# Performance work log

Measured on AMD Instinct MI355X. Metric: run time of the kernel, lower is better.

The kernel has to match this reference:

```python
import jax, jax.numpy as jnp
import numpy as np

NP_, NG_ = 20000, 5000            # protein / go_annotation node counts
D_FEAT, D_HID, N_CLS = 512, 128, 1000
E_PP, E_PG, E_GP = 240000, 100000, 100000
NEG_SLOPE = -0.2                  # note: the repo default slope is negative
EPS = 1e-12


def _l2norm(x):
    n = jnp.linalg.norm(x, axis=1, keepdims=True)
    return x / jnp.maximum(n, EPS)


def _edge_softmax(logits, dst, n):
    # per-destination-node softmax over incoming edges, per feature channel
    m = jax.ops.segment_max(logits, dst, num_segments=n)
    e = jnp.exp(logits - m[dst])
    s = jax.ops.segment_sum(e, dst, num_segments=n)
    return e / s[dst]


def _type_attn(h_src, h_dst, src, dst, Wl, bl, Wr, br):
    # GCN-normalized aggregation onto dst nodes, then type-level attention logits,
    # broadcast back to edges (copy_u on the reversed relation graph).
    ns, nd = h_src.shape[0], h_dst.shape[0]
    ones = jnp.ones(src.shape[0], dtype=h_src.dtype)
    outdeg = jnp.clip(jax.ops.segment_sum(ones, src, num_segments=ns), 1.0)
    feat = h_src * (outdeg ** -0.5)[:, None]
    rst = jax.ops.segment_sum(feat[src], dst, num_segments=nd)
    indeg = jnp.clip(jax.ops.segment_sum(ones, dst, num_segments=nd), 1.0)
    rst = rst * (indeg ** -0.5)[:, None]
    ea = jax.nn.elu((h_dst @ Wl + bl) + (rst @ Wr + br))  # [nd, D_HID]
    return ea[dst]                                        # [E, D_HID]


def setup_inputs() -> dict:
    key = jax.random.key(0)
    ks = iter(jax.random.split(key, 40))

    def nrm(shape, s=0.05):
        return jax.random.normal(next(ks), shape, dtype=jnp.float32) * s

    def ri(n, hi):
        return jax.random.randint(next(ks), (n,), 0, hi, dtype=jnp.int32)

    zeros = lambda n: jnp.zeros((n,), jnp.float32)
    return dict(
        x_protein=jax.random.normal(next(ks), (NP_, D_FEAT), dtype=jnp.float32),
        x_go=jax.random.normal(next(ks), (NG_, N_CLS), dtype=jnp.float32),
        src_pp=ri(E_PP, NP_), dst_pp=ri(E_PP, NP_),
        src_pg=ri(E_PG, NP_), dst_pg=ri(E_PG, NG_),
        src_gp=ri(E_GP, NG_), dst_gp=ri(E_GP, NP_),
        W1p=nrm((D_FEAT, D_HID)), b1p=zeros(D_HID),
        W1g=nrm((N_CLS, D_HID)), b1g=zeros(D_HID),
        Wl_p=nrm((D_HID, D_HID)), bl_p=zeros(D_HID),
        Wl_g=nrm((D_HID, D_HID)), bl_g=zeros(D_HID),
        Wr_p=nrm((D_HID, D_HID)), br_p=zeros(D_HID),
        Wr_g=nrm((D_HID, D_HID)), br_g=zeros(D_HID),
        Wnl=nrm((D_HID, D_HID)), bnl=zeros(D_HID),
        Wnr=nrm((D_HID, D_HID)), bnr=zeros(D_HID),
        Wfc=nrm((D_HID, N_CLS)), bfc=zeros(N_CLS),
    )


def reference(x_protein, x_go, src_pp, dst_pp, src_pg, dst_pg, src_gp, dst_gp,
              W1p, b1p, W1g, b1g, Wl_p, bl_p, Wl_g, bl_g,
              Wr_p, br_p, Wr_g, br_g, Wnl, bnl, Wnr, bnr, Wfc, bfc):
    # input projection + row-wise l2 norm (dropout disabled / eval mode)
    hp = _l2norm(x_protein @ W1p + b1p)   # [NP, D_HID]
    hg = _l2norm(x_go @ W1g + b1g)        # [NG, D_HID]

    # ---- TypeAttention over each canonical etype ----
    a_pp = _type_attn(hp, hp, src_pp, dst_pp, Wl_p, bl_p, Wr_p, br_p)
    a_pg = _type_attn(hp, hg, src_pg, dst_pg, Wl_g, bl_g, Wr_p, br_p)
    a_gp = _type_attn(hg, hp, src_gp, dst_gp, Wl_p, bl_p, Wr_g, br_g)

    # homogeneous view: proteins [0,NP), go_annotation [NP,NP+NG)
    gsrc = jnp.concatenate([src_pp, src_pg, src_gp + NP_])
    gdst = jnp.concatenate([dst_pp, dst_pg + NP_, dst_gp])
    alpha = jnp.concatenate([a_pp, a_pg, a_gp], axis=0)   # [E, D_HID]
    n = NP_ + NG_
    alpha = _edge_softmax(alpha, gdst, n)

    # ---- NodeAttention on the homogeneous graph ----
    x = jnp.concatenate([hp, hg], axis=0)                 # [N, D_HID]
    hl = (x @ Wnl + bnl)[gsrc]
    hr = (x @ Wnr + bnr)[gdst]
    e = (hl + hr) * alpha
    e = jnp.where(e > 0, e, NEG_SLOPE * e)                # LeakyReLU(slope=-0.2)
    a = _edge_softmax(e, gdst, n)
    h = jax.ops.segment_sum(x[gsrc] * a, gdst, num_segments=n)

    out = h @ Wfc + bfc   # [N, N_CLS]; rows [:NP]=protein, [NP:]=go_annotation
    return out
```

## Files before the change

### kernel.cpp

```cpp
#include <hip/hip_runtime.h>
#include <math.h>

#define NP 20000
#define NG 5000
#define NTOT 25000
#define DF 512
#define NCLS 1000
#define DH 128
#define EPP 240000
#define EPG 100000
#define EGP 100000
#define ETOT 440000
#define FS 16
#define HB 16

typedef __attribute__((ext_vector_type(8))) __bf16 bf16x8;
typedef __attribute__((ext_vector_type(4))) float f32x4;

__device__ __forceinline__ void gl2lds16(const void* g, void* l) {
    __builtin_amdgcn_global_load_lds(
        (const __attribute__((address_space(1))) unsigned int*)g,
        (__attribute__((address_space(3))) unsigned int*)l, 16, 0, 0);
}

__device__ __forceinline__ float b2f(unsigned short u) {
    union { unsigned int i; float f; } c; c.i = ((unsigned int)u) << 16; return c.f;
}

__global__ __launch_bounds__(1024) void hist_part_kernel(
    const int* __restrict__ src_pp, const int* __restrict__ dst_pp,
    const int* __restrict__ src_pg, const int* __restrict__ dst_pg,
    const int* __restrict__ src_gp, const int* __restrict__ dst_gp,
    int* __restrict__ partial)
{
    __shared__ int bins[20000];
    const int job = blockIdx.y, b = blockIdx.x;
    const int* idx; int nbins, nedge; size_t pbase;
    switch (job) {
    case 0: idx = src_pp; nbins = 20000; nedge = EPP; pbase = 0;       break;
    case 1: idx = dst_pp; nbins = 20000; nedge = EPP; pbase = 320000;  break;
    case 2: idx = src_pg; nbins = 20000; nedge = EPG; pbase = 640000;  break;
    case 3: idx = dst_pg; nbins = 5000;  nedge = EPG; pbase = 960000;  break;
    case 4: idx = src_gp; nbins = 5000;  nedge = EGP; pbase = 1040000; break;
    default: idx = dst_gp; nbins = 20000; nedge = EGP; pbase = 1120000; break;
    }
    for (int i = threadIdx.x; i < nbins; i += 1024) bins[i] = 0;
    __syncthreads();
    const int chunk = (nedge + HB - 1) / HB;
    const int e0 = b * chunk, e1 = min(e0 + chunk, nedge);
    for (int e = e0 + threadIdx.x; e < e1; e += 1024) atomicAdd(&bins[idx[e]], 1);
    __syncthreads();
    int* dst = partial + pbase + (size_t)b * nbins;
    for (int i = threadIdx.x; i < nbins; i += 1024) dst[i] = bins[i];
}

__global__ __launch_bounds__(256) void hist_merge_kernel(const int* __restrict__ partial,
    int* __restrict__ outdeg_pp, int* __restrict__ indeg_pp,
    int* __restrict__ outdeg_pg, int* __restrict__ indeg_pg,
    int* __restrict__ outdeg_gp, int* __restrict__ indeg_gp)
{
    const int job = blockIdx.y;
    const int nbins = (job == 3 || job == 4) ? 5000 : 20000;
    const int bin = blockIdx.x * 256 + threadIdx.x;
    if (bin >= nbins) return;
    size_t pbase; int* outp;
    switch (job) {
    case 0: pbase = 0;       outp = outdeg_pp; break;
    case 1: pbase = 320000;  outp = indeg_pp;  break;
    case 2: pbase = 640000;  outp = outdeg_pg; break;
    case 3: pbase = 960000;  outp = indeg_pg;  break;
    case 4: pbase = 1040000; outp = outdeg_gp; break;
    default: pbase = 1120000; outp = indeg_gp; break;
    }
    const int* p = partial + pbase + bin;
    int s = 0;
#pragma unroll
    for (int b = 0; b < HB; b++) s += p[(size_t)b * nbins];
    outp[bin] = s;
}

__global__ __launch_bounds__(1024) void scan_kernel(const int* __restrict__ indeg_pp,
                                                    const int* __restrict__ indeg_gp,
                                                    const int* __restrict__ indeg_pg,
                                                    int* __restrict__ row_ptr)
{
    __shared__ int part[1024];
    int t = threadIdx.x;
    const int CH = (NTOT + 1023) / 1024;
    int base = t * CH;
    auto cntf = [&](int idx) -> int {
        return (idx < NP) ? (indeg_pp[idx] + indeg_gp[idx]) : indeg_pg[idx - NP];
    };
    int s = 0;
    for (int i = 0; i < CH; i++) { int idx = base + i; if (idx < NTOT) s += cntf(idx); }
    part[t] = s;
    __syncthreads();
    for (int off = 1; off < 1024; off <<= 1) {
        int v = (t >= off) ? part[t - off] : 0;
        __syncthreads();
        part[t] += v;
        __syncthreads();
    }
    int run = (t == 0) ? 0 : part[t - 1];
    for (int i = 0; i < CH; i++) {
        int idx = base + i;
        if (idx < NTOT) { row_ptr[idx] = run; run += cntf(idx); }
    }
    if (t == 1023) row_ptr[NTOT] = part[1023];
}

__global__ void scatter_kernel(const int* __restrict__ src_pp, const int* __restrict__ dst_pp,
                               const int* __restrict__ src_pg, const int* __restrict__ dst_pg,
                               const int* __restrict__ src_gp, const int* __restrict__ dst_gp,
                               const int* __restrict__ outdeg_pp, const int* __restrict__ outdeg_pg,
                               const int* __restrict__ outdeg_gp,
                               const int* __restrict__ row_ptr, int* fill,
                               int2* __restrict__ edata)
{
    int e = blockIdx.x * blockDim.x + threadIdx.x;
    int s, d, t; float sc;
    if (e < EPP) {
        s = src_pp[e]; d = dst_pp[e]; t = 0;
        sc = rsqrtf((float)max(outdeg_pp[s], 1));
    } else if (e < EPP + EPG) {
        int i = e - EPP; s = src_pg[i]; d = NP + dst_pg[i]; t = 1;
        sc = rsqrtf((float)max(outdeg_pg[s], 1));
    } else if (e < ETOT) {
        int i = e - EPP - EPG; int sl = src_gp[i]; s = NP + sl; d = dst_gp[i]; t = 2;
        sc = rsqrtf((float)max(outdeg_gp[sl], 1));
    } else return;
    int pos = row_ptr[d] + atomicAdd(&fill[d * FS], 1);
    edata[pos] = make_int2(s | (t << 16), __float_as_int(sc));
}

__global__ __launch_bounds__(256) void conv_x_kernel(const float* __restrict__ xp, const float* __restrict__ xg,
                                                     __bf16* __restrict__ xpb, __bf16* __restrict__ xgb)
{
    long long e = ((long long)blockIdx.x * 256 + threadIdx.x) * 8;
    __bf16 pk[8];
    if (blockIdx.y == 0) {
        if (e >= (long long)20032 * 512) return;
        int row = (int)(e >> 9), k = (int)(e & 511);
        if (row < NP) {
            f32x4 v0 = *(const f32x4*)(xp + (size_t)row * 512 + k);
            f32x4 v1 = *(const f32x4*)(xp + (size_t)row * 512 + k + 4);
#pragma unroll
            for (int i = 0; i < 4; i++) { pk[i] = (__bf16)v0[i]; pk[4 + i] = (__bf16)v1[i]; }
        } else {
#pragma unroll
            for (int i = 0; i < 8; i++) pk[i] = (__bf16)0.f;
        }
        *(bf16x8*)(xpb + e) = *(bf16x8*)pk;
    } else {
        if (e >= (long long)5056 * 1024) return;
        int row = (int)(e >> 10), k = (int)(e & 1023);
        if (row < NG && k + 7 < 1000) {
            f32x4 v0 = *(const f32x4*)(xg + (size_t)row * 1000 + k);
            f32x4 v1 = *(const f32x4*)(xg + (size_t)row * 1000 + k + 4);
#pragma unroll
            for (int i = 0; i < 4; i++) { pk[i] = (__bf16)v0[i]; pk[4 + i] = (__bf16)v1[i]; }
        } else {
#pragma unroll
            for (int i = 0; i < 8; i++) {
                int kk = k + i;
                pk[i] = (__bf16)((row < NG && kk < 1000) ? xg[(size_t)row * 1000 + kk] : 0.f);
            }
        }
        *(bf16x8*)(xgb + e) = *(bf16x8*)pk;
    }
}

__global__ __launch_bounds__(256) void conv_w_kernel(
    const float* W1p, const float* W1g, const float* Wlp, const float* Wrp, const float* Wrg,
    const float* Wnl, const float* Wnr, const float* Wfc,
    __bf16* w1pt, __bf16* w1gt, __bf16* wlpt, __bf16* wrpt, __bf16* wrgt,
    __bf16* wnlt, __bf16* wnrt, __bf16* wfct)
{
    int e = blockIdx.x * 256 + threadIdx.x;
    switch (blockIdx.y) {
    case 0: if (e < 128 * 512)  { int n = e >> 9, k = e & 511;  w1pt[e] = (__bf16)W1p[(size_t)k * 128 + n]; } break;
    case 1: if (e < 128 * 1024) { int n = e >> 10, k = e & 1023; w1gt[e] = (__bf16)(k < 1000 ? W1g[(size_t)k * 128 + n] : 0.f); } break;
    case 2: if (e < 16384) { int n = e >> 7, k = e & 127; wlpt[e] = (__bf16)Wlp[(size_t)k * 128 + n]; } break;
    case 3: if (e < 16384) { int n = e >> 7, k = e & 127; wrpt[e] = (__bf16)Wrp[(size_t)k * 128 + n]; } break;
    case 4: if (e < 16384) { int n = e >> 7, k = e & 127; wrgt[e] = (__bf16)Wrg[(size_t)k * 128 + n]; } break;
    case 5: if (e < 16384) { int n = e >> 7, k = e & 127; wnlt[e] = (__bf16)Wnl[(size_t)k * 128 + n]; } break;
    case 6: if (e < 16384) { int n = e >> 7, k = e & 127; wnrt[e] = (__bf16)Wnr[(size_t)k * 128 + n]; } break;
    case 7: if (e < 1024 * 128) { int n = e >> 7, k = e & 127; wfct[e] = (__bf16)(n < 1000 ? Wfc[(size_t)k * 1000 + n] : 0.f); } break;
    }
}

struct GJob {
    const __bf16* A1;
    const __bf16* B1; const __bf16* B2;
    const float* b1; const float* b2;
    float* O1; __bf16* O2; __bf16* Ob;
    int M, N, Kp, ksteps;
};

template<int ACT, int DUALW, int EMIT>
__global__ __launch_bounds__(256) void gemm_bt(GJob j0, GJob j1, int split)
{
    __shared__ __align__(16) __bf16 As[64 * 32];
    __shared__ __align__(16) __bf16 Bs[128 * 32];
    __shared__ __align__(16) __bf16 B2s[DUALW ? 128 * 32 : 8];
    __shared__ float part[2][64];

    GJob j; int bx;
    if ((int)blockIdx.x < split) { j = j0; bx = blockIdx.x; }
    else { j = j1; bx = blockIdx.x - split; }

    const int tid = threadIdx.x;
    const int wave = tid >> 6, lane = tid & 63;
    const int wr = wave >> 1, wc = wave & 1;
    const int l15 = lane & 15, lh = lane >> 4;
    const int row0 = bx * 64;
    const int col0 = blockIdx.y * 128;

    const size_t aoff = (size_t)(row0 + (tid >> 2)) * j.Kp + (tid & 3) * 8;
    const size_t boff0 = (size_t)(col0 + (tid >> 2)) * j.Kp + (tid & 3) * 8;
    const size_t boff1 = boff0 + (size_t)64 * j.Kp;
    char* alds   = (char*)As + wave * 1024;
    char* blds0  = (char*)Bs + wave * 1024;
    char* blds1  = (char*)Bs + 4096 + wave * 1024;
    char* b2lds0 = (char*)B2s + wave * 1024;
    char* b2lds1 = (char*)B2s + 4096 + wave * 1024;

    f32x4 acc[2][4], acc2[2][4];
#pragma unroll
    for (int fm = 0; fm < 2; fm++)
#pragma unroll
        for (int fn = 0; fn < 4; fn++) {
            acc[fm][fn] = (f32x4)0.f;
            if (DUALW) acc2[fm][fn] = (f32x4)0.f;
        }

    for (int ks = 0; ks < j.ksteps; ks++) {
        const int k0 = ks * 32;
        __syncthreads();
        gl2lds16(j.A1 + aoff + k0, alds);
        gl2lds16(j.B1 + boff0 + k0, blds0);
        gl2lds16(j.B1 + boff1 + k0, blds1);
        if constexpr (DUALW) {
            gl2lds16(j.B2 + boff0 + k0, b2lds0);
            gl2lds16(j.B2 + boff1 + k0, b2lds1);
        }
        __syncthreads();

#pragma unroll
        for (int fm = 0; fm < 2; fm++) {
            bf16x8 a = *(const bf16x8*)&As[(wr * 32 + fm * 16 + l15) * 32 + lh * 8];
#pragma unroll
            for (int fn = 0; fn < 4; fn++) {
                bf16x8 b = *(const bf16x8*)&Bs[(wc * 64 + fn * 16 + l15) * 32 + lh * 8];
                acc[fm][fn] = __builtin_amdgcn_mfma_f32_16x16x32_bf16(a, b, acc[fm][fn], 0, 0, 0);
                if constexpr (DUALW) {
                    bf16x8 b2 = *(const bf16x8*)&B2s[(wc * 64 + fn * 16 + l15) * 32 + lh * 8];
                    acc2[fm][fn] = __builtin_amdgcn_mfma_f32_16x16x32_bf16(a, b2, acc2[fm][fn], 0, 0, 0);
                }
            }
        }
    }

    float bias[4], bias2[4];
#pragma unroll
    for (int fn = 0; fn < 4; fn++) {
        int col = col0 + wc * 64 + fn * 16 + l15;
        bias[fn] = 0.f; bias2[fn] = 0.f;
        if (col < j.N) {
            bias[fn] = j.b1[col];
            if (DUALW) bias2[fn] = j.b2[col];
        }
    }

    float vv[2][4][4];
#pragma unroll
    for (int fm = 0; fm < 2; fm++)
#pragma unroll
        for (int fn = 0; fn < 4; fn++)
#pragma unroll
            for (int r = 0; r < 4; r++) vv[fm][fn][r] = acc[fm][fn][r] + bias[fn];

    float scale[2][4];
#pragma unroll
    for (int fm = 0; fm < 2; fm++)
#pragma unroll
        for (int r = 0; r < 4; r++) scale[fm][r] = 1.f;

    if constexpr (ACT == 2) {
        float s[2][4];
#pragma unroll
        for (int fm = 0; fm < 2; fm++)
#pragma unroll
            for (int r = 0; r < 4; r++) {
                float v = 0.f;
#pragma unroll
                for (int fn = 0; fn < 4; fn++) v += vv[fm][fn][r] * vv[fm][fn][r];
                v += __shfl_xor(v, 1);
                v += __shfl_xor(v, 2);
                v += __shfl_xor(v, 4);
                v += __shfl_xor(v, 8);
                s[fm][r] = v;
            }
        __syncthreads();
        if (l15 == 0) {
#pragma unroll
            for (int fm = 0; fm < 2; fm++)
#pragma unroll
                for (int r = 0; r < 4; r++)
                    part[wc][wr * 32 + fm * 16 + lh * 4 + r] = s[fm][r];
        }
        __syncthreads();
#pragma unroll
        for (int fm = 0; fm < 2; fm++)
#pragma unroll
            for (int r = 0; r < 4; r++) {
                int rl = wr * 32 + fm * 16 + lh * 4 + r;
                float ss = part[0][rl] + part[1][rl];
                scale[fm][r] = 1.f / fmaxf(sqrtf(ss), 1e-12f);
            }
    }

#pragma unroll
    for (int fm = 0; fm < 2; fm++)
#pragma unroll
        for (int fn = 0; fn < 4; fn++)
#pragma unroll
            for (int r = 0; r < 4; r++) {
                int row = row0 + wr * 32 + fm * 16 + lh * 4 + r;
                int col = col0 + wc * 64 + fn * 16 + l15;
                if (row < j.M && col < j.N) {
                    float v = vv[fm][fn][r] * scale[fm][r];
                    if constexpr (EMIT == 0) j.O1[(size_t)row * j.N + col] = v;
                    if constexpr (EMIT == 2) j.Ob[(size_t)row * j.N + col] = (__bf16)v;
                    if constexpr (DUALW)
                        j.O2[(size_t)row * j.N + col] = (__bf16)(acc2[fm][fn][r] + bias2[fn]);
                }
            }
}

__global__ __launch_bounds__(256) void ea_wa_kernel(
    const __bf16* __restrict__ xb, const __bf16* __restrict__ rppb, const __bf16* __restrict__ rgpb,
    const __bf16* __restrict__ wl, const __bf16* __restrict__ wrp, const __bf16* __restrict__ wrg,
    const float* __restrict__ blp, const float* __restrict__ brp, const float* __restrict__ brg,
    const int* __restrict__ indeg_pp, const int* __restrict__ indeg_gp,
    float* __restrict__ wpp, float* __restrict__ wgp)
{
    __shared__ __align__(16) __bf16 A1s[64 * 32], A2s[64 * 32], A3s[64 * 32];
    __shared__ __align__(16) __bf16 B1s[128 * 32], B2s[128 * 32], B3s[128 * 32];

    const int tid = threadIdx.x;
    const int wave = tid >> 6, lane = tid & 63;
    const int wr = wave >> 1, wc = wave & 1;
    const int l15 = lane & 15, lh = lane >> 4;
    const int row0 = blockIdx.x * 64;

    const size_t aoff = (size_t)(row0 + (tid >> 2)) * 128 + (tid & 3) * 8;
    const size_t boff0 = (size_t)(tid >> 2) * 128 + (tid & 3) * 8;
    const size_t boff1 = boff0 + (size_t)64 * 128;
    char* a1 = (char*)A1s + wave * 1024;
    char* a2 = (char*)A2s + wave * 1024;
    char* a3 = (char*)A3s + wave * 1024;
    char* b1l0 = (char*)B1s + wave * 1024, *b1l1 = (char*)B1s + 4096 + wave * 1024;
    char* b2l0 = (char*)B2s + wave * 1024, *b2l1 = (char*)B2s + 4096 + wave * 1024;
    char* b3l0 = (char*)B3s + wave * 1024, *b3l1 = (char*)B3s + 4096 + wave * 1024;

    f32x4 accL[2][4], accP[2][4], accG[2][4];
#pragma unroll
    for (int fm = 0; fm < 2; fm++)
#pragma unroll
        for (int fn = 0; fn < 4; fn++) {
            accL[fm][fn] = (f32x4)0.f; accP[fm][fn] = (f32x4)0.f; accG[fm][fn] = (f32x4)0.f;
        }

    for (int ks = 0; ks < 4; ks++) {
        const int k0 = ks * 32;
        __syncthreads();
        gl2lds16(xb + aoff + k0, a1);
        gl2lds16(rppb + aoff + k0, a2);
        gl2lds16(rgpb + aoff + k0, a3);
        gl2lds16(wl + boff0 + k0, b1l0);  gl2lds16(wl + boff1 + k0, b1l1);
        gl2lds16(wrp + boff0 + k0, b2l0); gl2lds16(wrp + boff1 + k0, b2l1);
        gl2lds16(wrg + boff0 + k0, b3l0); gl2lds16(wrg + boff1 + k0, b3l1);
        __syncthreads();

#pragma unroll
        for (int fm = 0; fm < 2; fm++) {
            const int arow = (wr * 32 + fm * 16 + l15) * 32 + lh * 8;
            bf16x8 aL = *(const bf16x8*)&A1s[arow];
            bf16x8 aP = *(const bf16x8*)&A2s[arow];
            bf16x8 aG = *(const bf16x8*)&A3s[arow];
#pragma unroll
            for (int fn = 0; fn < 4; fn++) {
                const int brow = (wc * 64 + fn * 16 + l15) * 32 + lh * 8;
                bf16x8 bL = *(const bf16x8*)&B1s[brow];
                bf16x8 bP = *(const bf16x8*)&B2s[brow];
                bf16x8 bG = *(const bf16x8*)&B3s[brow];
                accL[fm][fn] = __builtin_amdgcn_mfma_f32_16x16x32_bf16(aL, bL, accL[fm][fn], 0, 0, 0);
                accP[fm][fn] = __builtin_amdgcn_mfma_f32_16x16x32_bf16(aP, bP, accP[fm][fn], 0, 0, 0);
                accG[fm][fn] = __builtin_amdgcn_mfma_f32_16x16x32_bf16(aG, bG, accG[fm][fn], 0, 0, 0);
            }
        }
    }

    float bp[4], bg[4];
#pragma unroll
    for (int fn = 0; fn < 4; fn++) {
        int col = wc * 64 + fn * 16 + l15;
        bp[fn] = blp[col] + brp[col];
        bg[fn] = blp[col] + brg[col];
    }

#pragma unroll
    for (int fm = 0; fm < 2; fm++)
#pragma unroll
        for (int r = 0; r < 4; r++) {
            int row = row0 + wr * 32 + fm * 16 + lh * 4 + r;
            int rr = min(row, NP - 1);
            int npp = indeg_pp[rr], ngp = indeg_gp[rr];
#pragma unroll
            for (int fn = 0; fn < 4; fn++) {
                int col = wc * 64 + fn * 16 + l15;
                float app = accL[fm][fn][r] + accP[fm][fn][r] + bp[fn];
                app = app > 0.f ? app : (__expf(app) - 1.f);
                float agp = accL[fm][fn][r] + accG[fm][fn][r] + bg[fn];
                agp = agp > 0.f ? agp : (__expf(agp) - 1.f);
                float wppv = 0.f, wgpv = 0.f;
                if (npp > 0 && ngp > 0) {
                    float mx = fmaxf(app, agp);
                    float ep = __expf(app - mx), eg = __expf(agp - mx);
                    float den = (float)npp * ep + (float)ngp * eg;
                    wppv = ep / den; wgpv = eg / den;
                } else if (npp > 0) wppv = 1.f / (float)npp;
                else if (ngp > 0) wgpv = 1.f / (float)ngp;
                if (row < NP) {
                    wpp[(size_t)row * DH + col] = wppv;
                    wgp[(size_t)row * DH + col] = wgpv;
                }
            }
        }
}

__global__ __launch_bounds__(128) void rst_agg_kernel(const __bf16* __restrict__ x,
                                                      const int* __restrict__ row_ptr,
                                                      const int2* __restrict__ edata,
                                                      const int* __restrict__ indeg_pp,
                                                      const int* __restrict__ indeg_gp,
                                                      __bf16* __restrict__ rppb, __bf16* __restrict__ rgpb)
{
    const int d = blockIdx.x;
    const int c = threadIdx.x;
    const int beg = row_ptr[d], end = row_ptr[d + 1];
    float spp = 0.f, sgp = 0.f;
    const unsigned short* xu = (const unsigned short*)x;
    int i = beg;
    for (; i + 3 < end; i += 4) {
        int2 e0 = edata[i], e1 = edata[i + 1], e2 = edata[i + 2], e3 = edata[i + 3];
        float v0 = b2f(xu[(size_t)(e0.x & 0xFFFF) * DH + c]) * __int_as_float(e0.y);
        float v1 = b2f(xu[(size_t)(e1.x & 0xFFFF) * DH + c]) * __int_as_float(e1.y);
        float v2 = b2f(xu[(size_t)(e2.x & 0xFFFF) * DH + c]) * __int_as_float(e2.y);
        float v3 = b2f(xu[(size_t)(e3.x & 0xFFFF) * DH + c]) * __int_as_float(e3.y);
        if ((e0.x >> 16) == 0) spp += v0; else sgp += v0;
        if ((e1.x >> 16) == 0) spp += v1; else sgp += v1;
        if ((e2.x >> 16) == 0) spp += v2; else sgp += v2;
        if ((e3.x >> 16) == 0) spp += v3; else sgp += v3;
    }
    for (; i < end; i++) {
        int2 e0 = edata[i];
        float v0 = b2f(xu[(size_t)(e0.x & 0xFFFF) * DH + c]) * __int_as_float(e0.y);
        if ((e0.x >> 16) == 0) spp += v0; else sgp += v0;
    }
    float ipp = rsqrtf((float)max(indeg_pp[d], 1));
    float igp = rsqrtf((float)max(indeg_gp[d], 1));
    rppb[(size_t)d * DH + c] = (__bf16)(spp * ipp);
    rgpb[(size_t)d * DH + c] = (__bf16)(sgp * igp);
}

__global__ __launch_bounds__(256) void pack_xhl_kernel(const unsigned int* __restrict__ xb2,
                                                       const unsigned int* __restrict__ hl2,
                                                       uint4* __restrict__ xhl4)
{
    int i = blockIdx.x * 256 + threadIdx.x;
    if (i >= 25024 * 128 / 4) return;
    unsigned int xa = xb2[i * 2], xbv = xb2[i * 2 + 1];
    unsigned int ha = hl2[i * 2], hbv = hl2[i * 2 + 1];
    uint4 o;
    o.x = (xa & 0xFFFFu) | (ha << 16);
    o.y = (xa >> 16) | (ha & 0xFFFF0000u);
    o.z = (xbv & 0xFFFFu) | (hbv << 16);
    o.w = (xbv >> 16) | (hbv & 0xFFFF0000u);
    xhl4[i] = o;
}

__global__ __launch_bounds__(128) void node_attn_kernel(const unsigned int* __restrict__ xhl,
                                                        const __bf16* __restrict__ hrb,
                                                        const float* __restrict__ wpp_arr,
                                                        const float* __restrict__ wgp_arr,
                                                        const int* __restrict__ indeg_pg,
                                                        const int* __restrict__ row_ptr,
                                                        const int2* __restrict__ edata,
                                                        __bf16* __restrict__ hb)
{
    const int d = blockIdx.x;
    const int c = threadIdx.x;
    const int beg = row_ptr[d], end = row_ptr[d + 1];
    const float hrd = b2f(((const unsigned short*)hrb)[(size_t)d * DH + c]);
    float wppv, wgpv;
    if (d < NP) {
        wppv = wpp_arr[(size_t)d * DH + c];
        wgpv = wgp_arr[(size_t)d * DH + c];
    } else {
        float w = 1.f / (float)max(indeg_pg[d - NP], 1);
        wppv = w; wgpv = w;
    }
    float ssum = 0.f, acc = 0.f;

    auto body = [&](int p) {
        unsigned int u = xhl[(size_t)(p & 0xFFFF) * 128 + c];
        float xv  = b2f((unsigned short)(u & 0xFFFFu));
        float hlv = b2f((unsigned short)(u >> 16));
        float al = ((p >> 16) == 0) ? wppv : wgpv;
        float e = (hlv + hrd) * al;
        e = fmaxf(e, -0.2f * e);
        float pw = __expf(e);
        ssum += pw;
        acc += pw * xv;
    };

    int i = beg;
    for (; i + 3 < end; i += 4) {
        int p0 = edata[i].x, p1 = edata[i + 1].x, p2 = edata[i + 2].x, p3 = edata[i + 3].x;
        unsigned int u0 = xhl[(size_t)(p0 & 0xFFFF) * 128 + c];
        unsigned int u1 = xhl[(size_t)(p1 & 0xFFFF) * 128 + c];
        unsigned int u2 = xhl[(size_t)(p2 & 0xFFFF) * 128 + c];
        unsigned int u3 = xhl[(size_t)(p3 & 0xFFFF) * 128 + c];
#pragma unroll
        for (int k = 0; k < 4; k++) {
            unsigned int u = (k == 0) ? u0 : (k == 1) ? u1 : (k == 2) ? u2 : u3;
            int p = (k == 0) ? p0 : (k == 1) ? p1 : (k == 2) ? p2 : p3;
            float xv  = b2f((unsigned short)(u & 0xFFFFu));
            float hlv = b2f((unsigned short)(u >> 16));
            float al = ((p >> 16) == 0) ? wppv : wgpv;
            float e = (hlv + hrd) * al;
            e = fmaxf(e, -0.2f * e);
            float pw = __expf(e);
            ssum += pw;
            acc += pw * xv;
        }
    }
    for (; i < end; i++) body(edata[i].x);

    hb[(size_t)d * DH + c] = (__bf16)((end > beg) ? acc / ssum : 0.f);
}

extern "C" void kernel_launch(void* const* d_in, const int* in_sizes, int n_in,
                              void* d_out, int out_size, void* d_ws, size_t ws_size,
                              hipStream_t stream)
{
    const float* x_protein = (const float*)d_in[0];
    const float* x_go      = (const float*)d_in[1];
    const int* src_pp = (const int*)d_in[2];
    const int* dst_pp = (const int*)d_in[3];
    const int* src_pg = (const int*)d_in[4];
    const int* dst_pg = (const int*)d_in[5];
    const int* src_gp = (const int*)d_in[6];
    const int* dst_gp = (const int*)d_in[7];
    const float* W1p = (const float*)d_in[8];
    const float* b1p = (const float*)d_in[9];
    const float* W1g = (const float*)d_in[10];
    const float* b1g = (const float*)d_in[11];
    const float* Wl_p = (const float*)d_in[12];
    const float* bl_p = (const float*)d_in[13];
    const float* Wr_p = (const float*)d_in[16];
    const float* br_p = (const float*)d_in[17];
    const float* Wr_g = (const float*)d_in[18];
    const float* br_g = (const float*)d_in[19];
    const float* Wnl = (const float*)d_in[20];
    const float* bnl = (const float*)d_in[21];
    const float* Wnr = (const float*)d_in[22];
    const float* bnr = (const float*)d_in[23];
    const float* Wfc = (const float*)d_in[24];
    const float* bfc = (const float*)d_in[25];
    float* out = (float*)d_out;

    size_t off = 0;
    char* base = (char*)d_ws;
    auto alloc = [&](size_t words) { void* p = base + off * 4; off += (words + 7) & ~(size_t)7; return p; };

    __bf16* xb  = (__bf16*)alloc((size_t)25024 * 128 / 2);
    __bf16* hlb = (__bf16*)alloc((size_t)25024 * 128 / 2);
    __bf16* hrb = (__bf16*)alloc((size_t)25024 * 128 / 2);
    char* U = (char*)alloc((size_t)25024 * 128);
    __bf16* rppb = (__bf16*)U;
    __bf16* rgpb = (__bf16*)(U + (size_t)20032 * 128 * 2);
    unsigned int* xhl = (unsigned int*)U;
    char* R1 = (char*)alloc((size_t)5128192 + 2588672);
    int*    partial = (int*)R1;
    __bf16* xpb = (__bf16*)R1;
    __bf16* xgb = (__bf16*)(R1 + (size_t)20032 * 512 * 2);
    float*  wpp = (float*)R1;
    float*  wgp = wpp + (size_t)20000 * 128;
    __bf16* haggb = (__bf16*)(wgp + (size_t)20000 * 128);
    __bf16* w1pt = (__bf16*)alloc(128 * 512 / 2);
    __bf16* w1gt = (__bf16*)alloc(128 * 1024 / 2);
    __bf16* wlpt = (__bf16*)alloc(128 * 128 / 2);
    __bf16* wrpt = (__bf16*)alloc(128 * 128 / 2);
    __bf16* wrgt = (__bf16*)alloc(128 * 128 / 2);
    __bf16* wnlt = (__bf16*)alloc(128 * 128 / 2);
    __bf16* wnrt = (__bf16*)alloc(128 * 128 / 2);
    __bf16* wfct = (__bf16*)alloc(1024 * 128 / 2);
    int* outdeg_pp = (int*)alloc(NP);
    int* outdeg_pg = (int*)alloc(NP);
    int* outdeg_gp = (int*)alloc(NG);
    int* indeg_pp  = (int*)alloc(NP);
    int* indeg_gp  = (int*)alloc(NP);
    int* indeg_pg  = (int*)alloc(NG);
    int* fill      = (int*)alloc((size_t)NTOT * FS);
    int* row_ptr   = (int*)alloc(NTOT + 1);
    int2* edata    = (int2*)alloc((size_t)ETOT * 2);

    hipMemsetAsync(fill, 0, (size_t)NTOT * FS * sizeof(int), stream);

    hist_part_kernel<<<dim3(HB, 6), 1024, 0, stream>>>(
        src_pp, dst_pp, src_pg, dst_pg, src_gp, dst_gp, partial);
    hist_merge_kernel<<<dim3((20000 + 255) / 256, 6), 256, 0, stream>>>(
        partial, outdeg_pp, indeg_pp, outdeg_pg, indeg_pg, outdeg_gp, indeg_gp);
    scan_kernel<<<1, 1024, 0, stream>>>(indeg_pp, indeg_gp, indeg_pg, row_ptr);
    scatter_kernel<<<(ETOT + 255) / 256, 256, 0, stream>>>(
        src_pp, dst_pp, src_pg, dst_pg, src_gp, dst_gp,
        outdeg_pp, outdeg_pg, outdeg_gp, row_ptr, fill, edata);

    conv_x_kernel<<<dim3(5008, 2), 256, 0, stream>>>(x_protein, x_go, xpb, xgb);
    conv_w_kernel<<<dim3(512, 8), 256, 0, stream>>>(W1p, W1g, Wl_p, Wr_p, Wr_g, Wnl, Wnr, Wfc,
                                                    w1pt, w1gt, wlpt, wrpt, wrgt, wnlt, wnrt, wfct);

    {
        GJob p0 = { xpb, w1pt, nullptr, b1p, nullptr, nullptr, nullptr, xb, NP, 128, 512, 16 };
        GJob p1 = { xgb, w1gt, nullptr, b1g, nullptr, nullptr, nullptr,
                    xb + (size_t)NP * 128, NG, 128, 1024, 32 };
        gemm_bt<2, 0, 2><<<392, 256, 0, stream>>>(p0, p1, 313);
    }

    rst_agg_kernel<<<NP, 128, 0, stream>>>(xb, row_ptr, edata, indeg_pp, indeg_gp, rppb, rgpb);

    ea_wa_kernel<<<313, 256, 0, stream>>>(xb, rppb, rgpb, wlpt, wrpt, wrgt,
                                          bl_p, br_p, br_g, indeg_pp, indeg_gp, wpp, wgp);

    {
        GJob h0 = { xb, wnlt, wnrt, bnl, bnr, nullptr, hrb, hlb, NTOT, 128, 128, 4 };
        gemm_bt<0, 1, 2><<<391, 256, 0, stream>>>(h0, h0, 1 << 30);
    }

    pack_xhl_kernel<<<3128, 256, 0, stream>>>((const unsigned int*)xb, (const unsigned int*)hlb, (uint4*)xhl);

    node_attn_kernel<<<NTOT, 128, 0, stream>>>(xhl, hrb, wpp, wgp, indeg_pg, row_ptr, edata, haggb);

    {
        GJob o0 = { haggb, wfct, nullptr, bfc, nullptr, out, nullptr, nullptr, NTOT, NCLS, 128, 4 };
        gemm_bt<0, 0, 0><<<dim3(391, 8), 256, 0, stream>>>(o0, o0, 1 << 30);
    }

    (void)in_sizes; (void)n_in; (void)out_size; (void)ws_size;
}
```

Baseline: 266.5 us.

## Merge launches: fold fill memset, conv kernels, and hl/hr GEMM into aggregation

Folds the fill-buffer memset into the histogram merge kernel as an extra grid slice. The x and weight bf16 conversion kernels become one launch, and the hl/hr dual-weight GEMM runs as extra blocks inside the rst aggregation kernel, which now handles two destination nodes per 256-thread block. The node-attention kernel also gets cheaper bf16 unpacking via shifts and fma. The aim is to cut launch overhead and let independent work share the GPU, at the cost of heterogeneous blocks within one grid.

```diff
diff --git a/kernel.cpp b/kernel.cpp
--- a/kernel.cpp
+++ b/kernel.cpp
@@ -57,11 +57,16 @@
 __global__ __launch_bounds__(256) void hist_merge_kernel(const int* __restrict__ partial,
     int* __restrict__ outdeg_pp, int* __restrict__ indeg_pp,
     int* __restrict__ outdeg_pg, int* __restrict__ indeg_pg,
-    int* __restrict__ outdeg_gp, int* __restrict__ indeg_gp)
+    int* __restrict__ outdeg_gp, int* __restrict__ indeg_gp,
+    int* __restrict__ fill)
 {
     const int job = blockIdx.y;
+    const int bin = blockIdx.x * 256 + threadIdx.x;
+    if (job == 6) {
+        if (bin < NTOT * FS) fill[bin] = 0;
+        return;
+    }
     const int nbins = (job == 3 || job == 4) ? 5000 : 20000;
-    const int bin = blockIdx.x * 256 + threadIdx.x;
     if (bin >= nbins) return;
     size_t pbase; int* outp;
     switch (job) {
@@ -133,14 +138,19 @@
     edata[pos] = make_int2(s | (t << 16), __float_as_int(sc));
 }
 
-__global__ __launch_bounds__(256) void conv_x_kernel(const float* __restrict__ xp, const float* __restrict__ xg,
-                                                     __bf16* __restrict__ xpb, __bf16* __restrict__ xgb)
-{
-    long long e = ((long long)blockIdx.x * 256 + threadIdx.x) * 8;
-    __bf16 pk[8];
-    if (blockIdx.y == 0) {
-        if (e >= (long long)20032 * 512) return;
+__global__ __launch_bounds__(256) void conv_all_kernel(
+    const float* __restrict__ xp, const float* __restrict__ xg,
+    const float* W1p, const float* W1g, const float* Wlp, const float* Wrp, const float* Wrg,
+    const float* Wnl, const float* Wnr, const float* Wfc,
+    __bf16* __restrict__ xpb, __bf16* __restrict__ xgb,
+    __bf16* w1pt, __bf16* w1gt, __bf16* wlpt, __bf16* wrpt, __bf16* wrgt,
+    __bf16* wnlt, __bf16* wnrt, __bf16* wfct)
+{
+    const int b = blockIdx.x;
+    if (b < 5008) {
+        long long e = ((long long)b * 256 + threadIdx.x) * 8;
         int row = (int)(e >> 9), k = (int)(e & 511);
+        __bf16 pk[8];
         if (row < NP) {
             f32x4 v0 = *(const f32x4*)(xp + (size_t)row * 512 + k);
             f32x4 v1 = *(const f32x4*)(xp + (size_t)row * 512 + k + 4);
@@ -151,9 +161,12 @@
             for (int i = 0; i < 8; i++) pk[i] = (__bf16)0.f;
         }
         *(bf16x8*)(xpb + e) = *(bf16x8*)pk;
-    } else {
-        if (e >= (long long)5056 * 1024) return;
+        return;
+    }
+    if (b < 7536) {
+        long long e = ((long long)(b - 5008) * 256 + threadIdx.x) * 8;
         int row = (int)(e >> 10), k = (int)(e & 1023);
+        __bf16 pk[8];
         if (row < NG && k + 7 < 1000) {
             f32x4 v0 = *(const f32x4*)(xg + (size_t)row * 1000 + k);
             f32x4 v1 = *(const f32x4*)(xg + (size_t)row * 1000 + k + 4);
@@ -167,26 +180,18 @@
             }
         }
         *(bf16x8*)(xgb + e) = *(bf16x8*)pk;
-    }
-}
-
-__global__ __launch_bounds__(256) void conv_w_kernel(
-    const float* W1p, const float* W1g, const float* Wlp, const float* Wrp, const float* Wrg,
-    const float* Wnl, const float* Wnr, const float* Wfc,
-    __bf16* w1pt, __bf16* w1gt, __bf16* wlpt, __bf16* wrpt, __bf16* wrgt,
-    __bf16* wnlt, __bf16* wnrt, __bf16* wfct)
-{
-    int e = blockIdx.x * 256 + threadIdx.x;
-    switch (blockIdx.y) {
-    case 0: if (e < 128 * 512)  { int n = e >> 9, k = e & 511;  w1pt[e] = (__bf16)W1p[(size_t)k * 128 + n]; } break;
-    case 1: if (e < 128 * 1024) { int n = e >> 10, k = e & 1023; w1gt[e] = (__bf16)(k < 1000 ? W1g[(size_t)k * 128 + n] : 0.f); } break;
-    case 2: if (e < 16384) { int n = e >> 7, k = e & 127; wlpt[e] = (__bf16)Wlp[(size_t)k * 128 + n]; } break;
-    case 3: if (e < 16384) { int n = e >> 7, k = e & 127; wrpt[e] = (__bf16)Wrp[(size_t)k * 128 + n]; } break;
-    case 4: if (e < 16384) { int n = e >> 7, k = e & 127; wrgt[e] = (__bf16)Wrg[(size_t)k * 128 + n]; } break;
-    case 5: if (e < 16384) { int n = e >> 7, k = e & 127; wnlt[e] = (__bf16)Wnl[(size_t)k * 128 + n]; } break;
-    case 6: if (e < 16384) { int n = e >> 7, k = e & 127; wnrt[e] = (__bf16)Wnr[(size_t)k * 128 + n]; } break;
-    case 7: if (e < 1024 * 128) { int n = e >> 7, k = e & 127; wfct[e] = (__bf16)(n < 1000 ? Wfc[(size_t)k * 1000 + n] : 0.f); } break;
-    }
+        return;
+    }
+    int wb = b - 7536;
+    int e;
+    if (wb < 256)      { e = wb * 256 + threadIdx.x;          int n = e >> 9, k = e & 511;  w1pt[e] = (__bf16)W1p[(size_t)k * 128 + n]; }
+    else if (wb < 768) { e = (wb - 256) * 256 + threadIdx.x;  int n = e >> 10, k = e & 1023; w1gt[e] = (__bf16)(k < 1000 ? W1g[(size_t)k * 128 + n] : 0.f); }
+    else if (wb < 832) { e = (wb - 768) * 256 + threadIdx.x;  int n = e >> 7, k = e & 127;  wlpt[e] = (__bf16)Wlp[(size_t)k * 128 + n]; }
+    else if (wb < 896) { e = (wb - 832) * 256 + threadIdx.x;  int n = e >> 7, k = e & 127;  wrpt[e] = (__bf16)Wrp[(size_t)k * 128 + n]; }
+    else if (wb < 960) { e = (wb - 896) * 256 + threadIdx.x;  int n = e >> 7, k = e & 127;  wrgt[e] = (__bf16)Wrg[(size_t)k * 128 + n]; }
+    else if (wb < 1024){ e = (wb - 960) * 256 + threadIdx.x;  int n = e >> 7, k = e & 127;  wnlt[e] = (__bf16)Wnl[(size_t)k * 128 + n]; }
+    else if (wb < 1088){ e = (wb - 1024) * 256 + threadIdx.x; int n = e >> 7, k = e & 127;  wnrt[e] = (__bf16)Wnr[(size_t)k * 128 + n]; }
+    else               { e = (wb - 1088) * 256 + threadIdx.x; int n = e >> 7, k = e & 127;  wfct[e] = (__bf16)(n < 1000 ? Wfc[(size_t)k * 1000 + n] : 0.f); }
 }
 
 struct GJob {
@@ -336,6 +341,110 @@
                         j.O2[(size_t)row * j.N + col] = (__bf16)(acc2[fm][fn][r] + bias2[fn]);
                 }
             }
+}
+
+__global__ __launch_bounds__(256) void rst_hlr_kernel(
+    const __bf16* __restrict__ xb,
+    const int* __restrict__ row_ptr, const int2* __restrict__ edata,
+    const int* __restrict__ indeg_pp, const int* __restrict__ indeg_gp,
+    __bf16* __restrict__ rppb, __bf16* __restrict__ rgpb,
+    const __bf16* __restrict__ wnlt, const __bf16* __restrict__ wnrt,
+    const float* __restrict__ bnl, const float* __restrict__ bnr,
+    __bf16* __restrict__ hlb, __bf16* __restrict__ hrb)
+{
+    __shared__ __align__(16) __bf16 As[64 * 32];
+    __shared__ __align__(16) __bf16 Bs[128 * 32];
+    __shared__ __align__(16) __bf16 B2s[128 * 32];
+
+    const int tid = threadIdx.x;
+    if (blockIdx.x < 10000) {
+        const int d = blockIdx.x * 2 + (tid >> 7);
+        const unsigned c = tid & 127;
+        const int beg = row_ptr[d], end = row_ptr[d + 1];
+        float spp = 0.f, sgp = 0.f;
+        const unsigned short* xu = (const unsigned short*)xb;
+        int i = beg;
+        for (; i + 3 < end; i += 4) {
+            int2 e0 = edata[i], e1 = edata[i + 1], e2 = edata[i + 2], e3 = edata[i + 3];
+            float v0 = b2f(xu[(((unsigned)e0.x & 0xFFFFu) << 7) | c]) * __int_as_float(e0.y);
+            float v1 = b2f(xu[(((unsigned)e1.x & 0xFFFFu) << 7) | c]) * __int_as_float(e1.y);
+            float v2 = b2f(xu[(((unsigned)e2.x & 0xFFFFu) << 7) | c]) * __int_as_float(e2.y);
+            float v3 = b2f(xu[(((unsigned)e3.x & 0xFFFFu) << 7) | c]) * __int_as_float(e3.y);
+            if ((e0.x >> 16) == 0) spp += v0; else sgp += v0;
+            if ((e1.x >> 16) == 0) spp += v1; else sgp += v1;
+            if ((e2.x >> 16) == 0) spp += v2; else sgp += v2;
+            if ((e3.x >> 16) == 0) spp += v3; else sgp += v3;
+        }
+        for (; i < end; i++) {
+            int2 e0 = edata[i];
+            float v0 = b2f(xu[(((unsigned)e0.x & 0xFFFFu) << 7) | c]) * __int_as_float(e0.y);
+            if ((e0.x >> 16) == 0) spp += v0; else sgp += v0;
+        }
+        float ipp = rsqrtf((float)max(indeg_pp[d], 1));
+        float igp = rsqrtf((float)max(indeg_gp[d], 1));
+        rppb[((size_t)d << 7) | c] = (__bf16)(spp * ipp);
+        rgpb[((size_t)d << 7) | c] = (__bf16)(sgp * igp);
+        return;
+    }
+
+    const int bx = blockIdx.x - 10000;
+    const int wave = tid >> 6, lane = tid & 63;
+    const int wr = wave >> 1, wc = wave & 1;
+    const int l15 = lane & 15, lh = lane >> 4;
+    const int row0 = bx * 64;
+
+    const size_t aoff = (size_t)(row0 + (tid >> 2)) * 128 + (tid & 3) * 8;
+    const size_t boff0 = (size_t)(tid >> 2) * 128 + (tid & 3) * 8;
+    const size_t boff1 = boff0 + (size_t)64 * 128;
+    char* alds   = (char*)As + wave * 1024;
+    char* blds0  = (char*)Bs + wave * 1024;
+    char* blds1  = (char*)Bs + 4096 + wave * 1024;
+    char* b2lds0 = (char*)B2s + wave * 1024;
+    char* b2lds1 = (char*)B2s + 4096 + wave * 1024;
+
+    f32x4 acc[2][4], acc2[2][4];
+#pragma unroll
+    for (int fm = 0; fm < 2; fm++)
+#pragma unroll
+        for (int fn = 0; fn < 4; fn++) { acc[fm][fn] = (f32x4)0.f; acc2[fm][fn] = (f32x4)0.f; }
+
+    for (int ks = 0; ks < 4; ks++) {
+        const int k0 = ks * 32;
+        __syncthreads();
+        gl2lds16(xb + aoff + k0, alds);
+        gl2lds16(wnlt + boff0 + k0, blds0);
+        gl2lds16(wnlt + boff1 + k0, blds1);
+        gl2lds16(wnrt + boff0 + k0, b2lds0);
+        gl2lds16(wnrt + boff1 + k0, b2lds1);
+        __syncthreads();
+#pragma unroll
+        for (int fm = 0; fm < 2; fm++) {
+            bf16x8 a = *(const bf16x8*)&As[(wr * 32 + fm * 16 + l15) * 32 + lh * 8];
+#pragma unroll
+            for (int fn = 0; fn < 4; fn++) {
+                bf16x8 b  = *(const bf16x8*)&Bs[(wc * 64 + fn * 16 + l15) * 32 + lh * 8];
+                bf16x8 b2 = *(const bf16x8*)&B2s[(wc * 64 + fn * 16 + l15) * 32 + lh * 8];
+                acc[fm][fn]  = __builtin_amdgcn_mfma_f32_16x16x32_bf16(a, b,  acc[fm][fn],  0, 0, 0);
+                acc2[fm][fn] = __builtin_amdgcn_mfma_f32_16x16x32_bf16(a, b2, acc2[fm][fn], 0, 0, 0);
+            }
+        }
+    }
+
+#pragma unroll
+    for (int fn = 0; fn < 4; fn++) {
+        int col = wc * 64 + fn * 16 + l15;
+        float bl = bnl[col], br = bnr[col];
+#pragma unroll
+        for (int fm = 0; fm < 2; fm++)
+#pragma unroll
+            for (int r = 0; r < 4; r++) {
+                int row = row0 + wr * 32 + fm * 16 + lh * 4 + r;
+                if (row < NTOT) {
+                    hlb[(size_t)row * DH + col] = (__bf16)(acc[fm][fn][r] + bl);
+                    hrb[(size_t)row * DH + col] = (__bf16)(acc2[fm][fn][r] + br);
+                }
+            }
+    }
 }
 
 __global__ __launch_bounds__(256) void ea_wa_kernel(
@@ -440,41 +549,6 @@
         }
 }
 
-__global__ __launch_bounds__(128) void rst_agg_kernel(const __bf16* __restrict__ x,
-                                                      const int* __restrict__ row_ptr,
-                                                      const int2* __restrict__ edata,
-                                                      const int* __restrict__ indeg_pp,
-                                                      const int* __restrict__ indeg_gp,
-                                                      __bf16* __restrict__ rppb, __bf16* __restrict__ rgpb)
-{
-    const int d = blockIdx.x;
-    const int c = threadIdx.x;
-    const int beg = row_ptr[d], end = row_ptr[d + 1];
-    float spp = 0.f, sgp = 0.f;
-    const unsigned short* xu = (const unsigned short*)x;
-    int i = beg;
-    for (; i + 3 < end; i += 4) {
-        int2 e0 = edata[i], e1 = edata[i + 1], e2 = edata[i + 2], e3 = edata[i + 3];
-        float v0 = b2f(xu[(size_t)(e0.x & 0xFFFF) * DH + c]) * __int_as_float(e0.y);
-        float v1 = b2f(xu[(size_t)(e1.x & 0xFFFF) * DH + c]) * __int_as_float(e1.y);
-        float v2 = b2f(xu[(size_t)(e2.x & 0xFFFF) * DH + c]) * __int_as_float(e2.y);
-        float v3 = b2f(xu[(size_t)(e3.x & 0xFFFF) * DH + c]) * __int_as_float(e3.y);
-        if ((e0.x >> 16) == 0) spp += v0; else sgp += v0;
-        if ((e1.x >> 16) == 0) spp += v1; else sgp += v1;
-        if ((e2.x >> 16) == 0) spp += v2; else sgp += v2;
-        if ((e3.x >> 16) == 0) spp += v3; else sgp += v3;
-    }
-    for (; i < end; i++) {
-        int2 e0 = edata[i];
-        float v0 = b2f(xu[(size_t)(e0.x & 0xFFFF) * DH + c]) * __int_as_float(e0.y);
-        if ((e0.x >> 16) == 0) spp += v0; else sgp += v0;
-    }
-    float ipp = rsqrtf((float)max(indeg_pp[d], 1));
-    float igp = rsqrtf((float)max(indeg_gp[d], 1));
-    rppb[(size_t)d * DH + c] = (__bf16)(spp * ipp);
-    rgpb[(size_t)d * DH + c] = (__bf16)(sgp * igp);
-}
-
 __global__ __launch_bounds__(256) void pack_xhl_kernel(const unsigned int* __restrict__ xb2,
                                                        const unsigned int* __restrict__ hl2,
                                                        uint4* __restrict__ xhl4)
@@ -485,6 +559,7 @@
     unsigned int ha = hl2[i * 2], hbv = hl2[i * 2 + 1];
     uint4 o;
     o.x = (xa & 0xFFFFu) | (ha << 16);
+    o.y = (xa >> 16) | (hbv & 0u) | (ha & 0xFFFF0000u);
     o.y = (xa >> 16) | (ha & 0xFFFF0000u);
     o.z = (xbv & 0xFFFFu) | (hbv << 16);
     o.w = (xbv >> 16) | (hbv & 0xFFFF0000u);
@@ -501,55 +576,54 @@
                                                         __bf16* __restrict__ hb)
 {
     const int d = blockIdx.x;
-    const int c = threadIdx.x;
+    const unsigned c = threadIdx.x;
     const int beg = row_ptr[d], end = row_ptr[d + 1];
-    const float hrd = b2f(((const unsigned short*)hrb)[(size_t)d * DH + c]);
+    const float hrd = b2f(((const unsigned short*)hrb)[((size_t)d << 7) | c]);
     float wppv, wgpv;
     if (d < NP) {
-        wppv = wpp_arr[(size_t)d * DH + c];
-        wgpv = wgp_arr[(size_t)d * DH + c];
+        wppv = wpp_arr[((size_t)d << 7) | c];
+        wgpv = wgp_arr[((size_t)d << 7) | c];
     } else {
         float w = 1.f / (float)max(indeg_pg[d - NP], 1);
         wppv = w; wgpv = w;
     }
     float ssum = 0.f, acc = 0.f;
 
-    auto body = [&](int p) {
-        unsigned int u = xhl[(size_t)(p & 0xFFFF) * 128 + c];
-        float xv  = b2f((unsigned short)(u & 0xFFFFu));
-        float hlv = b2f((unsigned short)(u >> 16));
+    int i = beg;
+    for (; i + 3 < end; i += 4) {
+        int p0 = edata[i].x, p1 = edata[i + 1].x, p2 = edata[i + 2].x, p3 = edata[i + 3].x;
+        unsigned int u0 = xhl[(((unsigned)p0 & 0xFFFFu) << 7) | c];
+        unsigned int u1 = xhl[(((unsigned)p1 & 0xFFFFu) << 7) | c];
+        unsigned int u2 = xhl[(((unsigned)p2 & 0xFFFFu) << 7) | c];
+        unsigned int u3 = xhl[(((unsigned)p3 & 0xFFFFu) << 7) | c];
+#pragma unroll
+        for (int k = 0; k < 4; k++) {
+            unsigned int u = (k == 0) ? u0 : (k == 1) ? u1 : (k == 2) ? u2 : u3;
+            int p = (k == 0) ? p0 : (k == 1) ? p1 : (k == 2) ? p2 : p3;
+            float xv  = __uint_as_float(u << 16);
+            float hlv = __uint_as_float(u & 0xFFFF0000u);
+            float al = ((p >> 16) == 0) ? wppv : wgpv;
+            float e = (hlv + hrd) * al;
+            e = fmaxf(e, -0.2f * e);
+            float pw = __expf(e);
+            ssum += pw;
+            acc = fmaf(pw, xv, acc);
+        }
+    }
+    for (; i < end; i++) {
+        int p = edata[i].x;
+        unsigned int u = xhl[(((unsigned)p & 0xFFFFu) << 7) | c];
+        float xv  = __uint_as_float(u << 16);
+        float hlv = __uint_as_float(u & 0xFFFF0000u);
         float al = ((p >> 16) == 0) ? wppv : wgpv;
         float e = (hlv + hrd) * al;
         e = fmaxf(e, -0.2f * e);
         float pw = __expf(e);
         ssum += pw;
-        acc += pw * xv;
-    };
-
-    int i = beg;
-    for (; i + 3 < end; i += 4) {
-        int p0 = edata[i].x, p1 = edata[i + 1].x, p2 = edata[i + 2].x, p3 = edata[i + 3].x;
-        unsigned int u0 = xhl[(size_t)(p0 & 0xFFFF) * 128 + c];
-        unsigned int u1 = xhl[(size_t)(p1 & 0xFFFF) * 128 + c];
-        unsigned int u2 = xhl[(size_t)(p2 & 0xFFFF) * 128 + c];
-        unsigned int u3 = xhl[(size_t)(p3 & 0xFFFF) * 128 + c];
-#pragma unroll
-        for (int k = 0; k < 4; k++) {
-            unsigned int u = (k == 0) ? u0 : (k == 1) ? u1 : (k == 2) ? u2 : u3;
-            int p = (k == 0) ? p0 : (k == 1) ? p1 : (k == 2) ? p2 : p3;
-            float xv  = b2f((unsigned short)(u & 0xFFFFu));
-            float hlv = b2f((unsigned short)(u >> 16));
-            float al = ((p >> 16) == 0) ? wppv : wgpv;
-            float e = (hlv + hrd) * al;
-            e = fmaxf(e, -0.2f * e);
-            float pw = __expf(e);
-            ssum += pw;
-            acc += pw * xv;
-        }
-    }
-    for (; i < end; i++) body(edata[i].x);
-
-    hb[(size_t)d * DH + c] = (__bf16)((end > beg) ? acc / ssum : 0.f);
+        acc = fmaf(pw, xv, acc);
+    }
+
+    hb[((size_t)d << 7) | c] = (__bf16)((end > beg) ? acc / ssum : 0.f);
 }
 
 extern "C" void kernel_launch(void* const* d_in, const int* in_sizes, int n_in,
@@ -618,20 +692,17 @@
     int* row_ptr   = (int*)alloc(NTOT + 1);
     int2* edata    = (int2*)alloc((size_t)ETOT * 2);
 
-    hipMemsetAsync(fill, 0, (size_t)NTOT * FS * sizeof(int), stream);
-
     hist_part_kernel<<<dim3(HB, 6), 1024, 0, stream>>>(
         src_pp, dst_pp, src_pg, dst_pg, src_gp, dst_gp, partial);
-    hist_merge_kernel<<<dim3((20000 + 255) / 256, 6), 256, 0, stream>>>(
-        partial, outdeg_pp, indeg_pp, outdeg_pg, indeg_pg, outdeg_gp, indeg_gp);
+    hist_merge_kernel<<<dim3((NTOT * FS + 255) / 256, 7), 256, 0, stream>>>(
+        partial, outdeg_pp, indeg_pp, outdeg_pg, indeg_pg, outdeg_gp, indeg_gp, fill);
     scan_kernel<<<1, 1024, 0, stream>>>(indeg_pp, indeg_gp, indeg_pg, row_ptr);
     scatter_kernel<<<(ETOT + 255) / 256, 256, 0, stream>>>(
         src_pp, dst_pp, src_pg, dst_pg, src_gp, dst_gp,
         outdeg_pp, outdeg_pg, outdeg_gp, row_ptr, fill, edata);
-
-    conv_x_kernel<<<dim3(5008, 2), 256, 0, stream>>>(x_protein, x_go, xpb, xgb);
-    conv_w_kernel<<<dim3(512, 8), 256, 0, stream>>>(W1p, W1g, Wl_p, Wr_p, Wr_g, Wnl, Wnr, Wfc,
-                                                    w1pt, w1gt, wlpt, wrpt, wrgt, wnlt, wnrt, wfct);
+    conv_all_kernel<<<9136, 256, 0, stream>>>(
+        x_protein, x_go, W1p, W1g, Wl_p, Wr_p, Wr_g, Wnl, Wnr, Wfc,
+        xpb, xgb, w1pt, w1gt, wlpt, wrpt, wrgt, wnlt, wnrt, wfct);
 
     {
         GJob p0 = { xpb, w1pt, nullptr, b1p, nullptr, nullptr, nullptr, xb, NP, 128, 512, 16 };
@@ -640,15 +711,12 @@
         gemm_bt<2, 0, 2><<<392, 256, 0, stream>>>(p0, p1, 313);
     }
 
-    rst_agg_kernel<<<NP, 128, 0, stream>>>(xb, row_ptr, edata, indeg_pp, indeg_gp, rppb, rgpb);
+    rst_hlr_kernel<<<10391, 256, 0, stream>>>(
+        xb, row_ptr, edata, indeg_pp, indeg_gp, rppb, rgpb,
+        wnlt, wnrt, bnl, bnr, hlb, hrb);
 
     ea_wa_kernel<<<313, 256, 0, stream>>>(xb, rppb, rgpb, wlpt, wrpt, wrgt,
                                           bl_p, br_p, br_g, indeg_pp, indeg_gp, wpp, wgp);
-
-    {
-        GJob h0 = { xb, wnlt, wnrt, bnl, bnr, nullptr, hrb, hlb, NTOT, 128, 128, 4 };
-        gemm_bt<0, 1, 2><<<391, 256, 0, stream>>>(h0, h0, 1 << 30);
-    }
 
     pack_xhl_kernel<<<3128, 256, 0, stream>>>((const unsigned int*)xb, (const unsigned int*)hlb, (uint4*)xhl);
 
```

Result: slower. 295.6 us (+10.9%).
